# Performance work log

Measured on AMD Instinct MI355X. Metric: run time of the kernel, lower is better.

Reference implementation:

```python
import jax, jax.numpy as jnp
import numpy as np
from jax import lax

NUM_OBJECTS = 3
KERNEL_DIM = 3
REDUCTION = 8


def setup_inputs() -> dict:
    key = jax.random.key(0)
    k1, k2, k3 = jax.random.split(key, 3)
    bs, C, h, w = 8, 256, 64, 64
    steps = 3
    f_e = jax.random.normal(k1, (bs, C, h, w), dtype=jnp.float32)
    # [steps, num_objects*k*k, bs, emb_dim]
    all_prototypes = jax.random.normal(k2, (steps, NUM_OBJECTS * KERNEL_DIM * KERNEL_DIM, bs, C), dtype=jnp.float32) * 0.05
    w_head = jax.random.normal(k3, (C,), dtype=jnp.float32) * 0.05
    b_head = jnp.zeros((1,), dtype=jnp.float32)
    return {"f_e": f_e, "all_prototypes": all_prototypes, "w_head": w_head, "b_head": b_head}


def reference(f_e, all_prototypes, w_head, b_head):
    bs, C, h, w = f_e.shape
    steps = all_prototypes.shape[0]
    no, k = NUM_OBJECTS, KERNEL_DIM
    pad = k // 2
    # tile f_e over objects -> single-batch multi-channel input, [1, bs*no*C, h, w]
    lhs = jnp.broadcast_to(f_e[:, None], (bs, no, C, h, w)).reshape(1, bs * no * C, h, w)
    groups = bs * no * C
    outs = []
    for i in range(steps):  # small fixed loop over iterative OPE steps
        # [no*k*k, bs, C] -> [bs, no, C, k, k]
        protos = (all_prototypes[i]
                  .transpose(1, 0, 2)
                  .reshape(bs, no, k, k, C)
                  .transpose(0, 1, 4, 2, 3))
        rhs = protos.reshape(groups, 1, k, k)
        # depthwise correlation, groups = bs*no*C (matches F.conv2d with groups)
        resp = lax.conv_general_dilated(
            lhs, rhs, window_strides=(1, 1), padding=[(pad, pad), (pad, pad)],
            feature_group_count=groups,
            dimension_numbers=("NCHW", "OIHW", "NCHW"),
        ).reshape(bs, no, C, h, w)
        # softmax over object axis, then softmax-weighted sum over objects
        sm = jax.nn.softmax(resp, axis=1)
        reduced = jnp.sum(sm * resp, axis=1)  # [bs, C, h, w]
        dmap = jax.nn.relu(jnp.einsum("bchw,c->bhw", reduced, w_head) + b_head[0])[:, None]
        up = jax.image.resize(dmap, (bs, 1, h * REDUCTION, w * REDUCTION), method="bilinear")
        outs.append(up)
    return jnp.stack(outs)  # [steps, bs, 1, H, W]; outs[-1] is final, rest aux
```

## Files before the change

kernel.cpp:

```cpp
#include <hip/hip_runtime.h>
#include <math.h>

#define STEPS 3
#define BS 8
#define NCH 256
#define H 64
#define W 64
#define UP 8
#define OH (H*UP)
#define OW (W*UP)
#define GB 32
#define CPB (NCH/GB)
#define CPW (CPB/4)
#define WREC 112
#define DMAP_FLOATS (STEPS*BS*H*W)
#define WT_FLOATS (BS*NCH*STEPS*WREC)
#define PREP_N (STEPS*28*BS*NCH)

typedef __attribute__((ext_vector_type(2))) float v2f;

__global__ __launch_bounds__(256) void loca_prep(
    const float* __restrict__ ap, const float* __restrict__ w_head,
    float* __restrict__ wt)
{
    int t = blockIdx.x * 256 + threadIdx.x;
    if (t >= PREP_N) return;
    int c = t & (NCH - 1);
    int r = t >> 8;
    int b = r & (BS - 1);
    r >>= 3;
    int j = r % 28;
    int i = r / 28;
    float4 v;
    if (j < 27) {
        v.x = ap[(((size_t)i * 27 + 0 * 9 + j) * BS + b) * NCH + c];
        v.y = ap[(((size_t)i * 27 + 1 * 9 + j) * BS + b) * NCH + c];
        v.z = ap[(((size_t)i * 27 + 2 * 9 + j) * BS + b) * NCH + c];
        v.w = 0.f;
    } else {
        v.x = w_head[c]; v.y = 0.f; v.z = 0.f; v.w = 0.f;
    }
    ((float4*)wt)[((size_t)b * NCH + c) * (STEPS * 28) + (size_t)i * 28 + j] = v;
}

__global__ __launch_bounds__(256) void loca_dmap(
    const float* __restrict__ f_e,
    const float* __restrict__ wt,
    float* __restrict__ partial)
{
    __shared__ float wlds[CPB * STEPS * WREC];
    __shared__ float red[4][STEPS][256];

    const int tid  = threadIdx.x;
    const int lane = tid & 63;
    const int wv   = tid >> 6;
    const int rb   = blockIdx.x;
    const int b    = blockIdx.y;
    const int g    = blockIdx.z;
    const int row  = rb * 4 + (lane >> 4);
    const int xg   = lane & 15;
    const int C0   = g * CPB;

    {
        const float4* src = (const float4*)(wt + ((size_t)b * NCH + C0) * (STEPS * WREC));
        float4* dst = (float4*)wlds;
        dst[tid] = src[tid];
        dst[tid + 256] = src[tid + 256];
        if (tid < 672 - 512) dst[tid + 512] = src[tid + 512];
    }

    const float m_m1 = (row > 0)     ? 1.f : 0.f;
    const float m_p1 = (row < H - 1) ? 1.f : 0.f;
    const int r_m1 = row > 0     ? row - 1 : 0;
    const int r_p1 = row < H - 1 ? row + 1 : H - 1;

    const int cw = C0 + wv * CPW;
    const float* fb = f_e + ((size_t)b * NCH + cw) * (H * W);

    float acc[STEPS][4] = {};

    float4 nm = ((const float4*)(fb + r_m1 * W))[xg];
    float4 n0 = ((const float4*)(fb + row  * W))[xg];
    float4 np = ((const float4*)(fb + r_p1 * W))[xg];

    __syncthreads();

    for (int cc = 0; cc < CPW; ++cc) {
        float4 vm = nm, v0 = n0, vp = np;
        if (cc + 1 < CPW) {
            const float* fc = fb + (cc + 1) * (H * W);
            nm = ((const float4*)(fc + r_m1 * W))[xg];
            n0 = ((const float4*)(fc + row  * W))[xg];
            np = ((const float4*)(fc + r_p1 * W))[xg];
        }
        vm.x *= m_m1; vm.y *= m_m1; vm.z *= m_m1; vm.w *= m_m1;
        vp.x *= m_p1; vp.y *= m_p1; vp.z *= m_p1; vp.w *= m_p1;

        float Lm = __shfl_up(vm.w, 1);
        float L0 = __shfl_up(v0.w, 1);
        float Lp = __shfl_up(vp.w, 1);
        float Rm = __shfl_down(vm.x, 1);
        float R0 = __shfl_down(v0.x, 1);
        float Rp = __shfl_down(vp.x, 1);
        if (xg == 0)  { Lm = 0.f; L0 = 0.f; Lp = 0.f; }
        if (xg == 15) { Rm = 0.f; R0 = 0.f; Rp = 0.f; }

        float am[6]  = {Lm, vm.x, vm.y, vm.z, vm.w, Rm};
        float a0[6]  = {L0, v0.x, v0.y, v0.z, v0.w, R0};
        float apv[6] = {Lp, vp.x, vp.y, vp.z, vp.w, Rp};

        const int lc = wv * CPW + cc;

        #pragma unroll
        for (int i = 0; i < STEPS; ++i) {
            const float4* wq = (const float4*)(wlds + ((size_t)lc * STEPS + i) * WREC);

            v2f  p01[4] = {v2f{0.f,0.f}, v2f{0.f,0.f}, v2f{0.f,0.f}, v2f{0.f,0.f}};
            float p2[4] = {0.f, 0.f, 0.f, 0.f};

            #pragma unroll
            for (int dy = 0; dy < 3; ++dy) {
                const float* arow = (dy == 0) ? am : (dy == 1) ? a0 : apv;
                #pragma unroll
                for (int dx = 0; dx < 3; ++dx) {
                    float4 q = wq[dy * 3 + dx];
                    v2f w01; w01.x = q.x; w01.y = q.y;
                    #pragma unroll
                    for (int k = 0; k < 4; ++k) {
                        float a = arow[k + dx];
                        v2f aa; aa.x = a; aa.y = a;
                        p01[k] = w01 * aa + p01[k];
                        p2[k]  = fmaf(a, q.z, p2[k]);
                    }
                }
            }

            const float wh = wq[27].x;
            #pragma unroll
            for (int k = 0; k < 4; ++k) {
                float r0 = p01[k].x, r1 = p01[k].y, r2 = p2[k];
                float e0 = __expf(r0);
                float e1 = __expf(r1);
                float e2 = __expf(r2);
                float num = fmaf(e0, r0, fmaf(e1, r1, e2 * r2));
                float den = e0 + e1 + e2;
#if __has_builtin(__builtin_amdgcn_rcpf)
                float redv = num * __builtin_amdgcn_rcpf(den);
#else
                float redv = num / den;
#endif
                acc[i][k] = fmaf(wh, redv, acc[i][k]);
            }
        }
    }

    const int px = (lane >> 4) * 64 + xg * 4;
    #pragma unroll
    for (int i = 0; i < STEPS; ++i) {
        float4 a; a.x = acc[i][0]; a.y = acc[i][1]; a.z = acc[i][2]; a.w = acc[i][3];
        *(float4*)&red[wv][i][px] = a;
    }
    __syncthreads();
    if (wv < STEPS) {
        const int i = wv;
        float4 s0 = *(const float4*)&red[0][i][px];
        float4 s1 = *(const float4*)&red[1][i][px];
        float4 s2 = *(const float4*)&red[2][i][px];
        float4 s3 = *(const float4*)&red[3][i][px];
        float4 s;
        s.x = (s0.x + s1.x) + (s2.x + s3.x);
        s.y = (s0.y + s1.y) + (s2.y + s3.y);
        s.z = (s0.z + s1.z) + (s2.z + s3.z);
        s.w = (s0.w + s1.w) + (s2.w + s3.w);
        *(float4*)&partial[(size_t)g * DMAP_FLOATS + ((size_t)(i * BS + b)) * (H * W)
                           + row * W + xg * 4] = s;
    }
}

__global__ __launch_bounds__(256) void loca_reduce(
    const float* __restrict__ partial, const float* __restrict__ b_head,
    float* __restrict__ dmap)
{
    const int t = blockIdx.x * 256 + threadIdx.x;
    const float4* p = (const float4*)partial;
    float4 s = p[t];
    #pragma unroll
    for (int g = 1; g < GB; ++g) {
        float4 q = p[(size_t)g * (DMAP_FLOATS / 4) + t];
        s.x += q.x; s.y += q.y; s.z += q.z; s.w += q.w;
    }
    const float bias = b_head[0];
    s.x = fmaxf(s.x + bias, 0.f);
    s.y = fmaxf(s.y + bias, 0.f);
    s.z = fmaxf(s.z + bias, 0.f);
    s.w = fmaxf(s.w + bias, 0.f);
    ((float4*)dmap)[t] = s;
}

__global__ __launch_bounds__(256) void loca_upsample(
    const float* __restrict__ dmap, float* __restrict__ out)
{
    const int idx  = blockIdx.x * 256 + threadIdx.x;
    const int gx   = idx & (OW / 4 - 1);
    const int rest = idx >> 7;
    const int Y    = rest & (OH - 1);
    const int ib   = rest >> 9;

    const float* d = dmap + (size_t)ib * H * W;

    float yin = (Y + 0.5f) * 0.125f - 0.5f;
    float fy0 = floorf(yin);
    int   iy  = (int)fy0;
    float fy  = yin - fy0;
    int y0c = min(max(iy, 0), H - 1);
    int y1c = min(max(iy + 1, 0), H - 1);
    const float* row0 = d + y0c * W;
    const float* row1 = d + y1c * W;

    float4 o;
    float* op = &o.x;
    #pragma unroll
    for (int j = 0; j < 4; ++j) {
        int X = gx * 4 + j;
        float xin = (X + 0.5f) * 0.125f - 0.5f;
        float fx0 = floorf(xin);
        int   ix  = (int)fx0;
        float fx  = xin - fx0;
        int x0c = min(max(ix, 0), W - 1);
        int x1c = min(max(ix + 1, 0), W - 1);
        float a00 = row0[x0c], a01 = row0[x1c];
        float a10 = row1[x0c], a11 = row1[x1c];
        float v0 = a00 + fx * (a01 - a00);
        float v1 = a10 + fx * (a11 - a10);
        op[j] = v0 + fy * (v1 - v0);
    }
    ((float4*)out)[idx] = o;
}

extern "C" void kernel_launch(void* const* d_in, const int* in_sizes, int n_in,
                              void* d_out, int out_size, void* d_ws, size_t ws_size,
                              hipStream_t stream) {
    const float* f_e    = (const float*)d_in[0];
    const float* ap     = (const float*)d_in[1];
    const float* w_head = (const float*)d_in[2];
    const float* b_head = (const float*)d_in[3];
    float* out     = (float*)d_out;
    float* wt      = (float*)d_ws;
    float* partial = wt + WT_FLOATS;
    float* dmap    = partial + (size_t)GB * DMAP_FLOATS;

    loca_prep<<<(PREP_N + 255) / 256, 256, 0, stream>>>(ap, w_head, wt);

    dim3 g1(16, BS, GB);
    loca_dmap<<<g1, 256, 0, stream>>>(f_e, wt, partial);

    loca_reduce<<<DMAP_FLOATS / 4 / 256, 256, 0, stream>>>(partial, b_head, dmap);

    const int groups = STEPS * BS * OH * OW / 4;
    loca_upsample<<<groups / 256, 256, 0, stream>>>(dmap, out);
}
```

Measured before the change: 129.3 us.

## Split dmap work across waves by rows instead of channels, drop LDS reduction

Each wave in the dmap kernel now handles its own 4 rows across all channels of the group, rather than all 4 waves sharing the same rows and splitting channels. This removes the shared-memory cross-wave reduction and its second barrier, and cuts the grid from 16 to 4 row-blocks per batch and group. Each block now loads the LDS weights once per 16 rows instead of once per 4. The trade-off is four times fewer blocks, 1024 in total, with each wave running a longer serial channel loop, which may reduce latency hiding.

```diff
diff --git a/kernel.cpp b/kernel.cpp
--- a/kernel.cpp
+++ b/kernel.cpp
@@ -11,7 +11,6 @@
 #define OW (W*UP)
 #define GB 32
 #define CPB (NCH/GB)
-#define CPW (CPB/4)
 #define WREC 112
 #define DMAP_FLOATS (STEPS*BS*H*W)
 #define WT_FLOATS (BS*NCH*STEPS*WREC)
@@ -49,15 +48,14 @@
     float* __restrict__ partial)
 {
     __shared__ float wlds[CPB * STEPS * WREC];
-    __shared__ float red[4][STEPS][256];
 
     const int tid  = threadIdx.x;
     const int lane = tid & 63;
     const int wv   = tid >> 6;
-    const int rb   = blockIdx.x;
+    const int rg   = blockIdx.x;
     const int b    = blockIdx.y;
     const int g    = blockIdx.z;
-    const int row  = rb * 4 + (lane >> 4);
+    const int row  = rg * 16 + wv * 4 + (lane >> 4);
     const int xg   = lane & 15;
     const int C0   = g * CPB;
 
@@ -74,8 +72,7 @@
     const int r_m1 = row > 0     ? row - 1 : 0;
     const int r_p1 = row < H - 1 ? row + 1 : H - 1;
 
-    const int cw = C0 + wv * CPW;
-    const float* fb = f_e + ((size_t)b * NCH + cw) * (H * W);
+    const float* fb = f_e + ((size_t)b * NCH + C0) * (H * W);
 
     float acc[STEPS][4] = {};
 
@@ -85,9 +82,9 @@
 
     __syncthreads();
 
-    for (int cc = 0; cc < CPW; ++cc) {
+    for (int cc = 0; cc < CPB; ++cc) {
         float4 vm = nm, v0 = n0, vp = np;
-        if (cc + 1 < CPW) {
+        if (cc + 1 < CPB) {
             const float* fc = fb + (cc + 1) * (H * W);
             nm = ((const float4*)(fc + r_m1 * W))[xg];
             n0 = ((const float4*)(fc + row  * W))[xg];
@@ -109,11 +106,9 @@
         float a0[6]  = {L0, v0.x, v0.y, v0.z, v0.w, R0};
         float apv[6] = {Lp, vp.x, vp.y, vp.z, vp.w, Rp};
 
-        const int lc = wv * CPW + cc;
-
         #pragma unroll
         for (int i = 0; i < STEPS; ++i) {
-            const float4* wq = (const float4*)(wlds + ((size_t)lc * STEPS + i) * WREC);
+            const float4* wq = (const float4*)(wlds + ((size_t)cc * STEPS + i) * WREC);
 
             v2f  p01[4] = {v2f{0.f,0.f}, v2f{0.f,0.f}, v2f{0.f,0.f}, v2f{0.f,0.f}};
             float p2[4] = {0.f, 0.f, 0.f, 0.f};
@@ -154,24 +149,9 @@
         }
     }
 
-    const int px = (lane >> 4) * 64 + xg * 4;
     #pragma unroll
     for (int i = 0; i < STEPS; ++i) {
-        float4 a; a.x = acc[i][0]; a.y = acc[i][1]; a.z = acc[i][2]; a.w = acc[i][3];
-        *(float4*)&red[wv][i][px] = a;
-    }
-    __syncthreads();
-    if (wv < STEPS) {
-        const int i = wv;
-        float4 s0 = *(const float4*)&red[0][i][px];
-        float4 s1 = *(const float4*)&red[1][i][px];
-        float4 s2 = *(const float4*)&red[2][i][px];
-        float4 s3 = *(const float4*)&red[3][i][px];
-        float4 s;
-        s.x = (s0.x + s1.x) + (s2.x + s3.x);
-        s.y = (s0.y + s1.y) + (s2.y + s3.y);
-        s.z = (s0.z + s1.z) + (s2.z + s3.z);
-        s.w = (s0.w + s1.w) + (s2.w + s3.w);
+        float4 s; s.x = acc[i][0]; s.y = acc[i][1]; s.z = acc[i][2]; s.w = acc[i][3];
         *(float4*)&partial[(size_t)g * DMAP_FLOATS + ((size_t)(i * BS + b)) * (H * W)
                            + row * W + xg * 4] = s;
     }
@@ -251,7 +231,7 @@
 
     loca_prep<<<(PREP_N + 255) / 256, 256, 0, stream>>>(ap, w_head, wt);
 
-    dim3 g1(16, BS, GB);
+    dim3 g1(4, BS, GB);
     loca_dmap<<<g1, 256, 0, stream>>>(f_e, wt, partial);
 
     loca_reduce<<<DMAP_FLOATS / 4 / 256, 256, 0, stream>>>(partial, b_head, dmap);
```

Result: faster. 123.9 us (-4.2%).
